# Kernel tuning notes

Hardware: AMD Instinct MI355X
Metric: run time of the kernel (lower is better)

Reference implementation:

```python
import jax, jax.numpy as jnp
import numpy as np

N = 50000      # nodes
E = 800000     # directed edges (before self loops)
IN = 128       # in_channels
H = 4          # heads
C = 64         # hidden_channels per head
G = 64         # graphs in batch
SLOPE = 0.2    # PyG GATConv default negative_slope


def setup_inputs() -> dict:
    key = jax.random.key(0)
    ks = jax.random.split(key, 16)
    x = jax.random.normal(ks[0], (N, IN), jnp.float32)
    edge_index = jax.random.randint(ks[1], (2, E), 0, N, dtype=jnp.int32)
    batch = jnp.sort(jax.random.randint(ks[2], (N,), 0, G, dtype=jnp.int32))
    s_in = 1.0 / np.sqrt(IN)
    s_hid = 1.0 / np.sqrt(H * C)
    return {
        "x": x,
        "edge_index": edge_index,
        "batch": batch,
        # layer 1: GATConv(IN -> C, heads=H, concat)
        "W1": jax.random.normal(ks[3], (IN, H * C), jnp.float32) * s_in,
        "a_src1": jax.random.normal(ks[4], (H, C), jnp.float32) * s_hid,
        "a_dst1": jax.random.normal(ks[5], (H, C), jnp.float32) * s_hid,
        "b1": jnp.zeros((H * C,), jnp.float32),
        # layer 2: GATConv(H*C -> C, heads=H, concat)
        "W2": jax.random.normal(ks[6], (H * C, H * C), jnp.float32) * s_hid,
        "a_src2": jax.random.normal(ks[7], (H, C), jnp.float32) * s_hid,
        "a_dst2": jax.random.normal(ks[8], (H, C), jnp.float32) * s_hid,
        "b2": jnp.zeros((H * C,), jnp.float32),
        # classifier head
        "W_lin": jax.random.normal(ks[9], (H * C, 2), jnp.float32) * s_hid,
        "b_lin": jnp.zeros((2,), jnp.float32),
    }


def _gat_conv(x, src, dst, W, a_src, a_dst, b):
    """PyG-style GATConv (concat heads, self-loops already in src/dst)."""
    n = x.shape[0]
    h = (x @ W).reshape(n, H, C)                       # [n, H, C]
    alpha_s = jnp.einsum('nhc,hc->nh', h, a_src)       # [n, H]
    alpha_d = jnp.einsum('nhc,hc->nh', h, a_dst)
    e = alpha_s[src] + alpha_d[dst]                    # [Etot, H]
    e = jnp.where(e > 0, e, SLOPE * e)                 # LeakyReLU
    # segment softmax over edges incoming to each destination node
    e_max = jax.lax.stop_gradient(jax.ops.segment_max(e, dst, num_segments=n))
    ex = jnp.exp(e - e_max[dst])
    denom = jax.ops.segment_sum(ex, dst, num_segments=n)
    alpha = ex / denom[dst]                            # [Etot, H]
    msg = alpha[:, :, None] * h[src]                   # [Etot, H, C]
    out = jax.ops.segment_sum(msg, dst, num_segments=n)
    return out.reshape(n, H * C) + b


def reference(x, edge_index, batch, W1, a_src1, a_dst1, b1,
              W2, a_src2, a_dst2, b2, W_lin, b_lin):
    n = x.shape[0]
    # add self loops (PyG GATConv default add_self_loops=True)
    loop = jnp.arange(n, dtype=edge_index.dtype)
    src = jnp.concatenate([edge_index[0], loop])
    dst = jnp.concatenate([edge_index[1], loop])

    h = _gat_conv(x, src, dst, W1, a_src1, a_dst1, b1)
    h = jax.nn.elu(h)                                  # dropout inactive (eval)
    h = _gat_conv(h, src, dst, W2, a_src2, a_dst2, b2)
    h = jax.nn.elu(h)

    # global mean pool over node-to-graph assignment
    sums = jax.ops.segment_sum(h, batch, num_segments=G)
    cnt = jax.ops.segment_sum(jnp.ones((n,), h.dtype), batch, num_segments=G)
    pooled = sums / jnp.maximum(cnt, 1.0)[:, None]     # [G, H*C]

    return pooled @ W_lin + b_lin                      # [G, 2] logits
```

## Files before the change

kernel.cpp:

```cpp
#include <hip/hip_runtime.h>
#include <hip/hip_bf16.h>
#include <math.h>

#define NN 50000
#define EE 800000
#define IN_CH 128
#define HH 4
#define CC 64
#define GG 64
#define HC 256
#define SLOPE 0.2f

#define NBUK 98
#define BDST 512
#define CAPB 10240
#define CAPD 64

typedef short bf16x8 __attribute__((ext_vector_type(8)));
typedef float f32x4  __attribute__((ext_vector_type(4)));
typedef float f32x2  __attribute__((ext_vector_type(2)));

__device__ inline ushort f2bf(float f) {
    union { __hip_bfloat16 h; ushort u; } c;
    c.h = __float2bfloat16(f);
    return c.u;
}
__device__ inline float bfu(ushort u) {
    union { uint u; float f; } c; c.u = ((uint)u) << 16; return c.f;
}
__device__ inline uchar f2e4m3(float v) {
    return (uchar)(__builtin_amdgcn_cvt_pk_fp8_f32(v, v, 0, false) & 0xff);
}


__global__ void init_kernel(int* __restrict__ bcnt,
                            float* __restrict__ pool, float* __restrict__ pcnt) {
    int i = blockIdx.x * blockDim.x + threadIdx.x;
    if (i < NBUK) bcnt[i] = 0;
    if (i < GG * HC) pool[i] = 0.f;
    if (i < GG) pcnt[i] = 0.f;
}


__global__ __launch_bounds__(256) void partition_kernel(const int* __restrict__ ei,
                                                        int* __restrict__ bcnt,
                                                        int2* __restrict__ part,
                                                        int total) {
    __shared__ int hist[NBUK];
    __shared__ int base[NBUK];
    int t = threadIdx.x;
    int c0 = blockIdx.x * 2048;
    for (int b = t; b < NBUK; b += 256) hist[b] = 0;
    __syncthreads();
    int s[8], d[8], rk[8], bk[8];
    #pragma unroll
    for (int k = 0; k < 8; ++k) {
        int i = c0 + k * 256 + t;
        rk[k] = -1;
        if (i < total) {
            if (i < EE) { s[k] = ei[i]; d[k] = ei[EE + i]; }
            else        { s[k] = d[k] = i - EE; }
            bk[k] = d[k] >> 9;
            rk[k] = atomicAdd(&hist[bk[k]], 1);
        }
    }
    __syncthreads();
    for (int b = t; b < NBUK; b += 256) {
        int h = hist[b];
        base[b] = h ? atomicAdd(&bcnt[b], h) : 0;
    }
    __syncthreads();
    #pragma unroll
    for (int k = 0; k < 8; ++k) {
        if (rk[k] >= 0) {
            int pos = base[bk[k]] + rk[k];
            if (pos < CAPB)
                part[(size_t)bk[k] * CAPB + pos] = make_int2(s[k], d[k]);
        }
    }
}


__global__ __launch_bounds__(1024) void bucket_csr_kernel(const int* __restrict__ bcnt,
                                                          const int2* __restrict__ part,
                                                          ushort* __restrict__ csrb,
                                                          int* __restrict__ cnt_out, int n) {
    __shared__ int cnt[BDST];
    int b = blockIdx.x, t = threadIdx.x;
    int d0 = b << 9;
    for (int i = t; i < BDST; i += 1024) cnt[i] = 0;
    __syncthreads();
    int m = min(bcnt[b], CAPB);
    const int2* pp = part + (size_t)b * CAPB;
    for (int i = t; i < m; i += 1024) {
        int2 e = pp[i];
        int ld = e.y - d0;
        int r = atomicAdd(&cnt[ld], 1);
        if (r < CAPD)
            csrb[((size_t)(d0 + ld) << 6) + r] = (ushort)e.x;
    }
    __syncthreads();
    for (int i = t; i < BDST; i += 1024) {
        int dd = d0 + i;
        if (dd < n) cnt_out[dd] = min(cnt[i], CAPD);
    }
}


__global__ __launch_bounds__(256) void convert_w_kernel(const float* __restrict__ B,
                                                        ushort* __restrict__ Bt, int K) {
    __shared__ float tile[32][33];
    int kt = blockIdx.x;
    int n0 = blockIdx.y * 32;
    int tx = threadIdx.x & 31, ty = threadIdx.x >> 5;
    #pragma unroll
    for (int r = ty; r < 32; r += 8)
        tile[r][tx] = B[(size_t)(kt * 32 + r) * 256 + n0 + tx];
    __syncthreads();
    #pragma unroll
    for (int r = ty; r < 32; r += 8)
        Bt[((size_t)kt * 256 + n0 + r) * 32 + tx] = f2bf(tile[tx][r]);
}


template <int K, bool A_BF16>
__global__ __launch_bounds__(256) void mfma_gemm_fused(const void* __restrict__ Ap,
                                                       const ushort* __restrict__ Bt,
                                                       uchar* __restrict__ H8,
                                                       float* __restrict__ as_,
                                                       float* __restrict__ ad_,
                                                       const float* __restrict__ a_src,
                                                       const float* __restrict__ a_dst,
                                                       int M) {
    __shared__ __align__(16) ushort As[64 * 32];
    __shared__ __align__(16) ushort Bs[256 * 32];
    int tid = threadIdx.x;
    int wave = tid >> 6, lane = tid & 63;
    int bm = blockIdx.x * 64;

    f32x4 acc[4][4] = {{}};

    for (int k0 = 0; k0 < K; k0 += 32) {
        {
            int row = tid >> 2, sl = tid & 3;
            int gr = bm + row;
            uint4 q = {0u, 0u, 0u, 0u};
            if (gr < M) {
                if constexpr (A_BF16) {
                    q = *reinterpret_cast<const uint4*>((const ushort*)Ap + (size_t)gr * K + k0 + sl * 8);
                } else {
                    const float* ap = (const float*)Ap + (size_t)gr * K + k0 + sl * 8;
                    float4 f0 = *reinterpret_cast<const float4*>(ap);
                    float4 f1 = *reinterpret_cast<const float4*>(ap + 4);
                    q.x = (uint)f2bf(f0.x) | ((uint)f2bf(f0.y) << 16);
                    q.y = (uint)f2bf(f0.z) | ((uint)f2bf(f0.w) << 16);
                    q.z = (uint)f2bf(f1.x) | ((uint)f2bf(f1.y) << 16);
                    q.w = (uint)f2bf(f1.z) | ((uint)f2bf(f1.w) << 16);
                }
            }
            int ssl = sl ^ ((row >> 1) & 3);
            *reinterpret_cast<uint4*>(&As[row * 32 + ssl * 8]) = q;
        }
        {
            const ushort* bt = Bt + (size_t)(k0 >> 5) * (256 * 32);
            #pragma unroll
            for (int cI = 0; cI < 4; ++cI) {
                int idx = cI * 256 + tid;
                uint4 v = *reinterpret_cast<const uint4*>(bt + idx * 8);
                int n = idx >> 2, sl = idx & 3;
                int ssl = sl ^ ((n >> 1) & 3);
                *reinterpret_cast<uint4*>(&Bs[n * 32 + ssl * 8]) = v;
            }
        }
        __syncthreads();

        int r16 = lane & 15, kg = lane >> 4;
        bf16x8 af[4], bfr[4];
        #pragma unroll
        for (int mi = 0; mi < 4; ++mi) {
            int row = mi * 16 + r16;
            int ssl = kg ^ ((row >> 1) & 3);
            af[mi] = *reinterpret_cast<const bf16x8*>(&As[row * 32 + ssl * 8]);
        }
        #pragma unroll
        for (int ni = 0; ni < 4; ++ni) {
            int n = wave * 64 + ni * 16 + r16;
            int ssl = kg ^ ((n >> 1) & 3);
            bfr[ni] = *reinterpret_cast<const bf16x8*>(&Bs[n * 32 + ssl * 8]);
        }
        #pragma unroll
        for (int mi = 0; mi < 4; ++mi)
            #pragma unroll
            for (int ni = 0; ni < 4; ++ni)
                acc[mi][ni] = __builtin_amdgcn_mfma_f32_16x16x32_bf16(af[mi], bfr[ni], acc[mi][ni], 0, 0, 0);
        __syncthreads();
    }

    int r16 = lane & 15, rg = lane >> 4;
    float asv[4], adv[4];
    #pragma unroll
    for (int ni = 0; ni < 4; ++ni) {
        asv[ni] = a_src[wave * 64 + ni * 16 + r16];
        adv[ni] = a_dst[wave * 64 + ni * 16 + r16];
    }
    #pragma unroll
    for (int mi = 0; mi < 4; ++mi) {
        #pragma unroll
        for (int r = 0; r < 4; ++r) {
            int row = bm + mi * 16 + rg * 4 + r;
            float ps = 0.f, pd = 0.f;
            if (row < M) {
                #pragma unroll
                for (int ni = 0; ni < 4; ++ni) {
                    float v = acc[mi][ni][r];
                    H8[(size_t)row * HC + wave * 64 + ni * 16 + r16] = f2e4m3(v);
                    ps += v * asv[ni];
                    pd += v * adv[ni];
                }
            }
            #pragma unroll
            for (int o = 1; o < 16; o <<= 1) {
                ps += __shfl_xor(ps, o, 64);
                pd += __shfl_xor(pd, o, 64);
            }
            if (row < M && r16 == 0) {
                as_[row * HH + wave] = ps;
                ad_[row * HH + wave] = pd;
            }
        }
    }
}


template <bool OUT_BF16>
__global__ __launch_bounds__(256) void aggregate11_kernel(const uchar* __restrict__ h8,
                                                          const float* __restrict__ as_,
                                                          const float* __restrict__ ad_,
                                                          const int* __restrict__ cnt,
                                                          const ushort* __restrict__ csrb,
                                                          const float* __restrict__ bias,
                                                          void* __restrict__ outp, int n) {
    int w = threadIdx.x >> 6, lane = threadIdx.x & 63;
    int dst = blockIdx.x * 4 + w;
    if (dst >= n) return;
    int es = lane >> 2, hh = lane & 3;
    int ep = lane >> 5, cl = lane & 31;
    int hsel = cl >> 3;

    __shared__ float s_alpha[4][64][4];
    __shared__ int   s_row[4][64];

    int deg = cnt[dst];
    const ushort* srcs = csrb + ((size_t)dst << 6);
    float ad = ad_[dst * HH + hh];

    float acc[8] = {};
    const char* hb = (const char*)h8 + cl * 8;

    int ntile = (deg + 15) >> 4;

#define DECODE_FMA(vv, aa)                                              \
    {                                                                   \
        f32x2 f_;                                                       \
        f_ = __builtin_amdgcn_cvt_pk_f32_fp8((int)(vv).x, false);       \
        acc[0] += (aa) * f_.x; acc[1] += (aa) * f_.y;                   \
        f_ = __builtin_amdgcn_cvt_pk_f32_fp8((int)(vv).x, true);        \
        acc[2] += (aa) * f_.x; acc[3] += (aa) * f_.y;                   \
        f_ = __builtin_amdgcn_cvt_pk_f32_fp8((int)(vv).y, false);       \
        acc[4] += (aa) * f_.x; acc[5] += (aa) * f_.y;                   \
        f_ = __builtin_amdgcn_cvt_pk_f32_fp8((int)(vv).y, true);        \
        acc[6] += (aa) * f_.x; acc[7] += (aa) * f_.y;                   \
    }

    float ew[4]; int sw[4];
    float lm = -INFINITY;
    #pragma unroll
    for (int t = 0; t < 4; ++t) {
        int j = t * 16 + es;
        float e = -INFINITY; int s = 0;
        if (t < ntile && j < deg) {
            s = (int)srcs[j];
            e = as_[s * HH + hh] + ad;
            e = e > 0.f ? e : SLOPE * e;
        }
        ew[t] = e; sw[t] = s;
        lm = fmaxf(lm, e);
    }
    #pragma unroll
    for (int o = 4; o < 64; o <<= 1) lm = fmaxf(lm, __shfl_xor(lm, o, 64));
    float den = 0.f;
    #pragma unroll
    for (int t = 0; t < 4; ++t) {
        float wgt = __expf(ew[t] - lm);
        ew[t] = wgt; den += wgt;
    }
    #pragma unroll
    for (int o = 4; o < 64; o <<= 1) den += __shfl_xor(den, o, 64);
    float invden = 1.f / den;
    #pragma unroll
    for (int t = 0; t < 4; ++t) {
        int j = t * 16 + es;
        if (t < ntile && j < deg) {
            s_alpha[w][j][hh] = ew[t] * invden;
            if (hh == 0) s_row[w][j] = sw[t] << 8;
        }
    }
    for (int jj = 0; jj < deg; jj += 8) {
        uint2 v0, v1, v2, v3;
        float a0, a1, a2, a3;
        {
            int j = jj + 0 + ep; int jc = j < deg ? j : 0;
            a0 = j < deg ? s_alpha[w][jc][hsel] : 0.f;
            v0 = *reinterpret_cast<const uint2*>(hb + s_row[w][jc]);
        }
        {
            int j = jj + 2 + ep; int jc = j < deg ? j : 0;
            a1 = j < deg ? s_alpha[w][jc][hsel] : 0.f;
            v1 = *reinterpret_cast<const uint2*>(hb + s_row[w][jc]);
        }
        {
            int j = jj + 4 + ep; int jc = j < deg ? j : 0;
            a2 = j < deg ? s_alpha[w][jc][hsel] : 0.f;
            v2 = *reinterpret_cast<const uint2*>(hb + s_row[w][jc]);
        }
        {
            int j = jj + 6 + ep; int jc = j < deg ? j : 0;
            a3 = j < deg ? s_alpha[w][jc][hsel] : 0.f;
            v3 = *reinterpret_cast<const uint2*>(hb + s_row[w][jc]);
        }
        DECODE_FMA(v0, a0)
        DECODE_FMA(v1, a1)
        DECODE_FMA(v2, a2)
        DECODE_FMA(v3, a3)
    }
#undef DECODE_FMA

    float fin[4];
    #pragma unroll
    for (int k = 0; k < 4; ++k) {
        float send = ep ? acc[k] : acc[4 + k];
        float recv = __shfl_xor(send, 32, 64);
        fin[k] = (ep ? acc[4 + k] : acc[k]) + recv;
    }

    int ch = cl * 8 + ep * 4;
    const float4 b4 = *reinterpret_cast<const float4*>(bias + ch);
    float r0 = fin[0] + b4.x, r1 = fin[1] + b4.y, r2 = fin[2] + b4.z, r3 = fin[3] + b4.w;
    r0 = r0 > 0.f ? r0 : __expf(r0) - 1.f;
    r1 = r1 > 0.f ? r1 : __expf(r1) - 1.f;
    r2 = r2 > 0.f ? r2 : __expf(r2) - 1.f;
    r3 = r3 > 0.f ? r3 : __expf(r3) - 1.f;
    if constexpr (OUT_BF16) {
        uint2 q;
        q.x = (uint)f2bf(r0) | ((uint)f2bf(r1) << 16);
        q.y = (uint)f2bf(r2) | ((uint)f2bf(r3) << 16);
        *reinterpret_cast<uint2*>((ushort*)outp + (size_t)dst * HC + ch) = q;
    } else {
        *reinterpret_cast<float4*>((float*)outp + (size_t)dst * HC + ch) =
            make_float4(r0, r1, r2, r3);
    }
}


__global__ __launch_bounds__(256) void pool_kernel(const ushort* __restrict__ o,
                                                   const int* __restrict__ batch,
                                                   float* __restrict__ pool,
                                                   float* __restrict__ pcnt, int n) {
    int t = threadIdx.x;
    int start = blockIdx.x * 64;
    if (start >= n) return;
    int endn = min(start + 64, n);
    int g = batch[start];
    float acc = 0.f;
    int cnt = 0;
    for (int node = start; node < endn; ++node) {
        int gb = batch[node];
        if (gb != g) {
            atomicAdd(&pool[g * HC + t], acc);
            if (t == 0) atomicAdd(&pcnt[g], (float)cnt);
            acc = 0.f; cnt = 0; g = gb;
        }
        acc += bfu(o[(size_t)node * HC + t]);
        cnt++;
    }
    atomicAdd(&pool[g * HC + t], acc);
    if (t == 0) atomicAdd(&pcnt[g], (float)cnt);
}

__global__ __launch_bounds__(256) void head_kernel(const float* __restrict__ pool,
                                                   const float* __restrict__ pcnt,
                                                   const float* __restrict__ Wl,
                                                   const float* __restrict__ bl,
                                                   float* __restrict__ out) {
    int g = blockIdx.x;
    int t = threadIdx.x;
    float inv = 1.f / fmaxf(pcnt[g], 1.f);
    float p = pool[g * HC + t] * inv;
    float v0 = p * Wl[t * 2 + 0];
    float v1 = p * Wl[t * 2 + 1];
    #pragma unroll
    for (int o = 32; o > 0; o >>= 1) {
        v0 += __shfl_down(v0, o, 64);
        v1 += __shfl_down(v1, o, 64);
    }
    __shared__ float s0[4], s1[4];
    int wid = t >> 6, lane = t & 63;
    if (lane == 0) { s0[wid] = v0; s1[wid] = v1; }
    __syncthreads();
    if (t == 0) {
        out[g * 2 + 0] = s0[0] + s0[1] + s0[2] + s0[3] + bl[0];
        out[g * 2 + 1] = s1[0] + s1[1] + s1[2] + s1[3] + bl[1];
    }
}


extern "C" void kernel_launch(void* const* d_in, const int* in_sizes, int n_in,
                              void* d_out, int out_size, void* d_ws, size_t ws_size,
                              hipStream_t stream) {
    const float* x    = (const float*)d_in[0];
    const int*   ei   = (const int*)d_in[1];
    const int*   batch= (const int*)d_in[2];
    const float* W1   = (const float*)d_in[3];
    const float* as1  = (const float*)d_in[4];
    const float* ad1  = (const float*)d_in[5];
    const float* b1   = (const float*)d_in[6];
    const float* W2   = (const float*)d_in[7];
    const float* as2  = (const float*)d_in[8];
    const float* ad2  = (const float*)d_in[9];
    const float* b2   = (const float*)d_in[10];
    const float* Wl   = (const float*)d_in[11];
    const float* bl   = (const float*)d_in[12];
    float* out = (float*)d_out;

    char* ws = (char*)d_ws;
    size_t off_b = 0;
    auto alloc = [&](size_t bytes) -> void* {
        void* p = ws + off_b;
        off_b = (off_b + bytes + 255) & ~(size_t)255;
        return p;
    };
    uchar*  h8   = (uchar*)alloc((size_t)NN * HC);
    ushort* o1   = (ushort*)alloc((size_t)NN * HC * 2);
    ushort* o2   = (ushort*)alloc((size_t)NN * HC * 2);
    float*  as_  = (float*)alloc((size_t)NN * HH * 4);
    float*  ad_  = (float*)alloc((size_t)NN * HH * 4);
    int*    bcnt = (int*)alloc((size_t)NBUK * 4);
    int2*   part = (int2*)alloc((size_t)NBUK * CAPB * 8);
    ushort* csrb = (ushort*)alloc((size_t)NN * CAPD * 2);
    int*    cnt  = (int*)alloc((size_t)NN * 4);
    float*  pool = (float*)alloc((size_t)GG * HC * 4);
    float*  pcnt = (float*)alloc((size_t)GG * 4);
    ushort* Bt1  = (ushort*)alloc((size_t)HC * IN_CH * 2);
    ushort* Bt2  = (ushort*)alloc((size_t)HC * HC * 2);
    if (off_b > ws_size) return;

    const int TOTAL = EE + NN;

    init_kernel<<<(GG * HC + 255) / 256, 256, 0, stream>>>(bcnt, pool, pcnt);
    partition_kernel<<<(TOTAL + 2047) / 2048, 256, 0, stream>>>(ei, bcnt, part, TOTAL);
    bucket_csr_kernel<<<NBUK, 1024, 0, stream>>>(bcnt, part, csrb, cnt, NN);

    convert_w_kernel<<<dim3(IN_CH / 32, 8), 256, 0, stream>>>(W1, Bt1, IN_CH);
    convert_w_kernel<<<dim3(HC / 32, 8), 256, 0, stream>>>(W2, Bt2, HC);

    int gblocks = (NN + 63) / 64;
    int ablocks = (NN + 3) / 4;
    mfma_gemm_fused<IN_CH, false><<<gblocks, 256, 0, stream>>>(x, Bt1, h8, as_, ad_, as1, ad1, NN);
    aggregate11_kernel<true><<<ablocks, 256, 0, stream>>>(h8, as_, ad_, cnt, csrb, b1, o1, NN);
    mfma_gemm_fused<HC, true><<<gblocks, 256, 0, stream>>>(o1, Bt2, h8, as_, ad_, as2, ad2, NN);
    aggregate11_kernel<true><<<ablocks, 256, 0, stream>>>(h8, as_, ad_, cnt, csrb, b2, o2, NN);
    pool_kernel<<<(NN + 63) / 64, 256, 0, stream>>>(o2, batch, pool, pcnt, NN);
    head_kernel<<<GG, 256, 0, stream>>>(pool, pcnt, Wl, bl, out);
}
```

Baseline: 197.9 us.

## Widen aggregation gathers to 16-byte loads with software-pipelined prefetch

The edge aggregation kernel now has each lane load 16 fp8 channels (uint4) instead of 8, with four edges in flight per wave instead of two. The gather loop is software-pipelined: the next chunk of rows is loaded before the current one is decoded and accumulated. Partial sums are reduced across the four edge groups with two shuffle stages, and only one quarter of the lanes writes 16 outputs each. This aims to raise bytes per memory instruction and hide gather latency, at the cost of twice the accumulator registers, more shuffles and idle lanes in the epilogue.

```diff
diff --git a/kernel.cpp b/kernel.cpp
--- a/kernel.cpp
+++ b/kernel.cpp
@@ -233,7 +233,7 @@
 
 
 template <bool OUT_BF16>
-__global__ __launch_bounds__(256) void aggregate11_kernel(const uchar* __restrict__ h8,
+__global__ __launch_bounds__(256) void aggregate12_kernel(const uchar* __restrict__ h8,
                                                           const float* __restrict__ as_,
                                                           const float* __restrict__ ad_,
                                                           const int* __restrict__ cnt,
@@ -244,8 +244,8 @@
     int dst = blockIdx.x * 4 + w;
     if (dst >= n) return;
     int es = lane >> 2, hh = lane & 3;
-    int ep = lane >> 5, cl = lane & 31;
-    int hsel = cl >> 3;
+    int eg = lane >> 4, cq = lane & 15;
+    int hsel = cq >> 2;
 
     __shared__ float s_alpha[4][64][4];
     __shared__ int   s_row[4][64];
@@ -254,110 +254,135 @@
     const ushort* srcs = csrb + ((size_t)dst << 6);
     float ad = ad_[dst * HH + hh];
 
-    float acc[8] = {};
-    const char* hb = (const char*)h8 + cl * 8;
+    const char* hb = (const char*)h8 + cq * 16;
+    float acc[16] = {};
 
     int ntile = (deg + 15) >> 4;
 
-#define DECODE_FMA(vv, aa)                                              \
-    {                                                                   \
-        f32x2 f_;                                                       \
-        f_ = __builtin_amdgcn_cvt_pk_f32_fp8((int)(vv).x, false);       \
-        acc[0] += (aa) * f_.x; acc[1] += (aa) * f_.y;                   \
-        f_ = __builtin_amdgcn_cvt_pk_f32_fp8((int)(vv).x, true);        \
-        acc[2] += (aa) * f_.x; acc[3] += (aa) * f_.y;                   \
-        f_ = __builtin_amdgcn_cvt_pk_f32_fp8((int)(vv).y, false);       \
-        acc[4] += (aa) * f_.x; acc[5] += (aa) * f_.y;                   \
-        f_ = __builtin_amdgcn_cvt_pk_f32_fp8((int)(vv).y, true);        \
-        acc[6] += (aa) * f_.x; acc[7] += (aa) * f_.y;                   \
-    }
-
-    float ew[4]; int sw[4];
-    float lm = -INFINITY;
-    #pragma unroll
-    for (int t = 0; t < 4; ++t) {
-        int j = t * 16 + es;
-        float e = -INFINITY; int s = 0;
-        if (t < ntile && j < deg) {
-            s = (int)srcs[j];
-            e = as_[s * HH + hh] + ad;
-            e = e > 0.f ? e : SLOPE * e;
-        }
-        ew[t] = e; sw[t] = s;
-        lm = fmaxf(lm, e);
-    }
-    #pragma unroll
-    for (int o = 4; o < 64; o <<= 1) lm = fmaxf(lm, __shfl_xor(lm, o, 64));
-    float den = 0.f;
-    #pragma unroll
-    for (int t = 0; t < 4; ++t) {
-        float wgt = __expf(ew[t] - lm);
-        ew[t] = wgt; den += wgt;
-    }
-    #pragma unroll
-    for (int o = 4; o < 64; o <<= 1) den += __shfl_xor(den, o, 64);
-    float invden = 1.f / den;
-    #pragma unroll
-    for (int t = 0; t < 4; ++t) {
-        int j = t * 16 + es;
-        if (t < ntile && j < deg) {
-            s_alpha[w][j][hh] = ew[t] * invden;
-            if (hh == 0) s_row[w][j] = sw[t] << 8;
-        }
-    }
-    for (int jj = 0; jj < deg; jj += 8) {
-        uint2 v0, v1, v2, v3;
-        float a0, a1, a2, a3;
-        {
-            int j = jj + 0 + ep; int jc = j < deg ? j : 0;
-            a0 = j < deg ? s_alpha[w][jc][hsel] : 0.f;
-            v0 = *reinterpret_cast<const uint2*>(hb + s_row[w][jc]);
-        }
-        {
-            int j = jj + 2 + ep; int jc = j < deg ? j : 0;
-            a1 = j < deg ? s_alpha[w][jc][hsel] : 0.f;
-            v1 = *reinterpret_cast<const uint2*>(hb + s_row[w][jc]);
-        }
-        {
-            int j = jj + 4 + ep; int jc = j < deg ? j : 0;
-            a2 = j < deg ? s_alpha[w][jc][hsel] : 0.f;
-            v2 = *reinterpret_cast<const uint2*>(hb + s_row[w][jc]);
-        }
-        {
-            int j = jj + 6 + ep; int jc = j < deg ? j : 0;
-            a3 = j < deg ? s_alpha[w][jc][hsel] : 0.f;
-            v3 = *reinterpret_cast<const uint2*>(hb + s_row[w][jc]);
-        }
-        DECODE_FMA(v0, a0)
-        DECODE_FMA(v1, a1)
-        DECODE_FMA(v2, a2)
-        DECODE_FMA(v3, a3)
-    }
-#undef DECODE_FMA
-
-    float fin[4];
-    #pragma unroll
-    for (int k = 0; k < 4; ++k) {
-        float send = ep ? acc[k] : acc[4 + k];
-        float recv = __shfl_xor(send, 32, 64);
-        fin[k] = (ep ? acc[4 + k] : acc[k]) + recv;
-    }
-
-    int ch = cl * 8 + ep * 4;
-    const float4 b4 = *reinterpret_cast<const float4*>(bias + ch);
-    float r0 = fin[0] + b4.x, r1 = fin[1] + b4.y, r2 = fin[2] + b4.z, r3 = fin[3] + b4.w;
-    r0 = r0 > 0.f ? r0 : __expf(r0) - 1.f;
-    r1 = r1 > 0.f ? r1 : __expf(r1) - 1.f;
-    r2 = r2 > 0.f ? r2 : __expf(r2) - 1.f;
-    r3 = r3 > 0.f ? r3 : __expf(r3) - 1.f;
-    if constexpr (OUT_BF16) {
-        uint2 q;
-        q.x = (uint)f2bf(r0) | ((uint)f2bf(r1) << 16);
-        q.y = (uint)f2bf(r2) | ((uint)f2bf(r3) << 16);
-        *reinterpret_cast<uint2*>((ushort*)outp + (size_t)dst * HC + ch) = q;
-    } else {
-        *reinterpret_cast<float4*>((float*)outp + (size_t)dst * HC + ch) =
-            make_float4(r0, r1, r2, r3);
+    {
+        float ew[4]; int sw[4];
+        float lm = -INFINITY;
+        #pragma unroll
+        for (int t = 0; t < 4; ++t) {
+            int j = t * 16 + es;
+            float e = -INFINITY; int s = 0;
+            if (t < ntile && j < deg) {
+                s = (int)srcs[j];
+                e = as_[s * HH + hh] + ad;
+                e = e > 0.f ? e : SLOPE * e;
+            }
+            ew[t] = e; sw[t] = s;
+            lm = fmaxf(lm, e);
+        }
+        #pragma unroll
+        for (int o = 4; o < 64; o <<= 1) lm = fmaxf(lm, __shfl_xor(lm, o, 64));
+        float den = 0.f;
+        #pragma unroll
+        for (int t = 0; t < 4; ++t) {
+            float wgt = __expf(ew[t] - lm);
+            ew[t] = wgt; den += wgt;
+        }
+        #pragma unroll
+        for (int o = 4; o < 64; o <<= 1) den += __shfl_xor(den, o, 64);
+        float invden = 1.f / den;
+        #pragma unroll
+        for (int t = 0; t < 4; ++t) {
+            int j = t * 16 + es;
+            if (t < ntile && j < deg) {
+                s_alpha[w][j][hh] = ew[t] * invden;
+                if (hh == 0) s_row[w][j] = sw[t] << 8;
+            }
+        }
+    }
+
+#define LOADCHUNK(base, v0, v1, a0, a1)                                  \
+    {                                                                    \
+        int j_ = (base) + eg; int jc_ = j_ < deg ? j_ : 0;               \
+        a0 = j_ < deg ? s_alpha[w][jc_][hsel] : 0.f;                     \
+        v0 = *reinterpret_cast<const uint4*>(hb + s_row[w][jc_]);        \
+        j_ = (base) + 4 + eg; jc_ = j_ < deg ? j_ : 0;                   \
+        a1 = j_ < deg ? s_alpha[w][jc_][hsel] : 0.f;                     \
+        v1 = *reinterpret_cast<const uint4*>(hb + s_row[w][jc_]);        \
+    }
+
+#define FMA16(vv, aa)                                                    \
+    {                                                                    \
+        f32x2 f_;                                                        \
+        f_ = __builtin_amdgcn_cvt_pk_f32_fp8((int)(vv).x, false);        \
+        acc[0] += (aa) * f_.x;  acc[1] += (aa) * f_.y;                   \
+        f_ = __builtin_amdgcn_cvt_pk_f32_fp8((int)(vv).x, true);         \
+        acc[2] += (aa) * f_.x;  acc[3] += (aa) * f_.y;                   \
+        f_ = __builtin_amdgcn_cvt_pk_f32_fp8((int)(vv).y, false);        \
+        acc[4] += (aa) * f_.x;  acc[5] += (aa) * f_.y;                   \
+        f_ = __builtin_amdgcn_cvt_pk_f32_fp8((int)(vv).y, true);         \
+        acc[6] += (aa) * f_.x;  acc[7] += (aa) * f_.y;                   \
+        f_ = __builtin_amdgcn_cvt_pk_f32_fp8((int)(vv).z, false);        \
+        acc[8] += (aa) * f_.x;  acc[9] += (aa) * f_.y;                   \
+        f_ = __builtin_amdgcn_cvt_pk_f32_fp8((int)(vv).z, true);         \
+        acc[10] += (aa) * f_.x; acc[11] += (aa) * f_.y;                  \
+        f_ = __builtin_amdgcn_cvt_pk_f32_fp8((int)(vv).w, false);        \
+        acc[12] += (aa) * f_.x; acc[13] += (aa) * f_.y;                  \
+        f_ = __builtin_amdgcn_cvt_pk_f32_fp8((int)(vv).w, true);         \
+        acc[14] += (aa) * f_.x; acc[15] += (aa) * f_.y;                  \
+    }
+
+    {
+        uint4 vA0, vA1; float aA0, aA1;
+        LOADCHUNK(0, vA0, vA1, aA0, aA1)
+        int jj = 0;
+        for (; jj + 8 < deg; jj += 8) {
+            uint4 vB0, vB1; float aB0, aB1;
+            LOADCHUNK(jj + 8, vB0, vB1, aB0, aB1)
+            FMA16(vA0, aA0)
+            FMA16(vA1, aA1)
+            vA0 = vB0; vA1 = vB1; aA0 = aB0; aA1 = aB1;
+        }
+        FMA16(vA0, aA0)
+        FMA16(vA1, aA1)
+    }
+#undef LOADCHUNK
+#undef FMA16
+
+    #pragma unroll
+    for (int k = 0; k < 16; ++k) {
+        acc[k] += __shfl_xor(acc[k], 16, 64);
+        acc[k] += __shfl_xor(acc[k], 32, 64);
+    }
+
+    if (eg == 0) {
+        int ch = cq * 16;
+        float r[16];
+        #pragma unroll
+        for (int q = 0; q < 4; ++q) {
+            const float4 b4 = *reinterpret_cast<const float4*>(bias + ch + q * 4);
+            r[q * 4 + 0] = acc[q * 4 + 0] + b4.x;
+            r[q * 4 + 1] = acc[q * 4 + 1] + b4.y;
+            r[q * 4 + 2] = acc[q * 4 + 2] + b4.z;
+            r[q * 4 + 3] = acc[q * 4 + 3] + b4.w;
+        }
+        #pragma unroll
+        for (int k = 0; k < 16; ++k)
+            r[k] = r[k] > 0.f ? r[k] : __expf(r[k]) - 1.f;
+        if constexpr (OUT_BF16) {
+            uint4 q0, q1;
+            q0.x = (uint)f2bf(r[0])  | ((uint)f2bf(r[1])  << 16);
+            q0.y = (uint)f2bf(r[2])  | ((uint)f2bf(r[3])  << 16);
+            q0.z = (uint)f2bf(r[4])  | ((uint)f2bf(r[5])  << 16);
+            q0.w = (uint)f2bf(r[6])  | ((uint)f2bf(r[7])  << 16);
+            q1.x = (uint)f2bf(r[8])  | ((uint)f2bf(r[9])  << 16);
+            q1.y = (uint)f2bf(r[10]) | ((uint)f2bf(r[11]) << 16);
+            q1.z = (uint)f2bf(r[12]) | ((uint)f2bf(r[13]) << 16);
+            q1.w = (uint)f2bf(r[14]) | ((uint)f2bf(r[15]) << 16);
+            ushort* op = (ushort*)outp + (size_t)dst * HC + ch;
+            *reinterpret_cast<uint4*>(op) = q0;
+            *reinterpret_cast<uint4*>(op + 8) = q1;
+        } else {
+            float* op = (float*)outp + (size_t)dst * HC + ch;
+            #pragma unroll
+            for (int q = 0; q < 4; ++q)
+                *reinterpret_cast<float4*>(op + q * 4) =
+                    make_float4(r[q * 4 + 0], r[q * 4 + 1], r[q * 4 + 2], r[q * 4 + 3]);
+        }
     }
 }
 
@@ -466,9 +491,9 @@
     int gblocks = (NN + 63) / 64;
     int ablocks = (NN + 3) / 4;
     mfma_gemm_fused<IN_CH, false><<<gblocks, 256, 0, stream>>>(x, Bt1, h8, as_, ad_, as1, ad1, NN);
-    aggregate11_kernel<true><<<ablocks, 256, 0, stream>>>(h8, as_, ad_, cnt, csrb, b1, o1, NN);
+    aggregate12_kernel<true><<<ablocks, 256, 0, stream>>>(h8, as_, ad_, cnt, csrb, b1, o1, NN);
     mfma_gemm_fused<HC, true><<<gblocks, 256, 0, stream>>>(o1, Bt2, h8, as_, ad_, as2, ad2, NN);
-    aggregate11_kernel<true><<<ablocks, 256, 0, stream>>>(h8, as_, ad_, cnt, csrb, b2, o2, NN);
+    aggregate12_kernel<true><<<ablocks, 256, 0, stream>>>(h8, as_, ad_, cnt, csrb, b2, o2, NN);
     pool_kernel<<<(NN + 63) / 64, 256, 0, stream>>>(o2, batch, pool, pcnt, NN);
     head_kernel<<<GG, 256, 0, stream>>>(pool, pcnt, Wl, bl, out);
 }
```

Result: slower. 219.5 us (+10.9%).
